# Kernel optimization log

Measured on AMD Instinct MI355X. Metric: run time of the kernel, lower is better.

The kernel has to match this reference:

```python
import jax, jax.numpy as jnp
import numpy as np

# V:N:M sparsity config (n=2 kept of m=8 per vector-block; mask pattern [1,0,1,0,0,0,0,0])
M_BLK = 8
KEEP_OFFSETS = np.array([0, 2], dtype=np.int32)  # positions kept in each m-block
B, S, D_IN, D_OUT = 2, 8192, 4096, 4096
K_KEPT = D_IN // M_BLK * len(KEEP_OFFSETS)  # 1024


def _keep_idx():
    # column indices of the surviving weight entries (same for every output row)
    blocks = np.arange(D_IN // M_BLK, dtype=np.int32)[:, None] * M_BLK  # [D_IN/M,1]
    return jnp.asarray((blocks + KEEP_OFFSETS[None, :]).reshape(-1))   # [K_KEPT]


def setup_inputs() -> dict:
    key = jax.random.key(0)
    k1, k2, k3 = jax.random.split(key, 3)
    x = jax.random.normal(k1, (B, S, D_IN), dtype=jnp.float32)
    values = jax.random.normal(k2, (D_OUT, K_KEPT), dtype=jnp.float32) * 0.02
    bias = jax.random.normal(k3, (D_OUT,), dtype=jnp.float32) * 0.02
    return {"x": x, "values": values, "bias": bias}


def reference(x, values, bias):
    # Sparse SpMM: gather kept input features, dense GEMM with compressed values.
    # Equivalent to x @ (masked dense W).T + bias, without materializing W.
    keep = _keep_idx()               # [K_KEPT] int32, constant metadata
    xg = x[..., keep]                # [B,S,K_KEPT]
    out = jnp.einsum('bsk,nk->bsn', xg, values) + bias  # [B,S,D_OUT]
    return out
```

## Files before the change

kernel.cpp:

```cpp
#include <hip/hip_runtime.h>
#include <hip/hip_bf16.h>


#define M_TOTAL 16384
#define DIN     4096
#define KDIM    1024
#define NDIM    4096

typedef unsigned short u16;
typedef unsigned int   u32;
typedef __bf16 bf16x8 __attribute__((ext_vector_type(8)));
typedef float  f32x4  __attribute__((ext_vector_type(4)));

typedef const void __attribute__((address_space(1)))* gp_t;
typedef void __attribute__((address_space(3)))*       lp_t;

__device__ __forceinline__ u16 f2bf(float f) {
    u32 u = __float_as_uint(f);
    u += 0x7FFFu + ((u >> 16) & 1u);
    return (u16)(u >> 16);
}

__global__ void compact_x_kernel(const float* __restrict__ x,
                                 u32* __restrict__ xg, int nblk) {
    int i = blockIdx.x * blockDim.x + threadIdx.x;
    const int stride = gridDim.x * blockDim.x;
    for (; i < nblk; i += stride) {
        float4 v = *reinterpret_cast<const float4*>(x + (size_t)i * 8);
        xg[i] = (u32)f2bf(v.x) | ((u32)f2bf(v.z) << 16);
    }
}

__global__ void conv_vals_kernel(const float* __restrict__ v,
                                 uint2* __restrict__ vb, int n4) {
    int i = blockIdx.x * blockDim.x + threadIdx.x;
    const int stride = gridDim.x * blockDim.x;
    for (; i < n4; i += stride) {
        float4 f = *reinterpret_cast<const float4*>(v + (size_t)i * 4);
        uint2 o;
        o.x = (u32)f2bf(f.x) | ((u32)f2bf(f.y) << 16);
        o.y = (u32)f2bf(f.z) | ((u32)f2bf(f.w) << 16);
        vb[i] = o;
    }
}


#define LDSA(d, kh) (((d) * 2 + (kh)) * 16384)
#define LDSB(d, kh) (65536 + ((d) * 2 + (kh)) * 16384)

#define LOADA(d, kh, mh) { _Pragma("unroll") \
    for (int m_ = 0; m_ < 4; ++m_) \
        af[m_] = *(const bf16x8*)(lds + LDSA(d, kh) + (wr * 8 + (mh) * 4 + m_) * 1024 + fl_off); }

#define LOADB(d, kh) { _Pragma("unroll") \
    for (int n_ = 0; n_ < 4; ++n_) \
        bfr[n_] = *(const bf16x8*)(lds + LDSB(d, kh) + (wc * 4 + n_) * 1024 + fl_off); }

#define MFMA16(mh) { \
    __builtin_amdgcn_s_setprio(1); \
    _Pragma("unroll") for (int m_ = 0; m_ < 4; ++m_) \
    _Pragma("unroll") for (int n_ = 0; n_ < 4; ++n_) \
        acc[(mh) * 4 + m_][n_] = __builtin_amdgcn_mfma_f32_16x16x32_bf16( \
            af[m_], bfr[n_], acc[(mh) * 4 + m_][n_], 0, 0, 0); \
    __builtin_amdgcn_s_setprio(0); }

#define BAR() __builtin_amdgcn_s_barrier()
#define VMCNT6() asm volatile("s_waitcnt vmcnt(6)" ::: "memory")
#define VMCNT0() asm volatile("s_waitcnt vmcnt(0)" ::: "memory")

__global__ __launch_bounds__(512, 2) void gemm_kernel(
    const u16* __restrict__ A, const u16* __restrict__ Bv,
    const float* __restrict__ bias, float* __restrict__ C)
{
    __shared__ __align__(1024) char lds[131072];

    const int tid  = threadIdx.x;
    const int lane = tid & 63;
    const int wid  = tid >> 6;
    const int wr   = wid >> 2;
    const int wc   = wid & 3;
    const int lrow = lane & 15;
    const int lg   = lane >> 4;

    const int b   = blockIdx.x;
    const int swz = (b & 7) * 128 + (b >> 3);
    const int btm = swz >> 4;
    const int btn = swz & 15;

    const int st_r0 = wid * 16 + (lane >> 2);
    const int st_ck = ((lane & 3) * 8) ^ ((lane & 32) >> 1);
    const u16* Asrc = A  + (size_t)(btm * 256 + st_r0) * KDIM + st_ck;
    const u16* Bsrc = Bv + (size_t)(btn * 256 + st_r0) * KDIM + st_ck;
    const int dst0 = tid * 16;

    const int fl_off = lrow * 64 + ((lg * 16) ^ (((lrow >> 3) & 1) << 5));

    auto STAGE = [&](int s) {
        const int kt = s >> 2, j = s & 3;
        const int d = kt & 1, kh = (j >> 1) & 1;
        const int ko = kt * 64 + kh * 32;
        const u16* src = (j & 1) ? Bsrc : Asrc;
        const int base = ((j & 1) ? 65536 : 0) + (d * 2 + kh) * 16384;
        __builtin_amdgcn_global_load_lds((gp_t)(src + ko),
            (lp_t)(lds + base + dst0), 16, 0, 0);
        __builtin_amdgcn_global_load_lds((gp_t)(src + 128 * KDIM + ko),
            (lp_t)(lds + base + 8192 + dst0), 16, 0, 0);
    };

    f32x4 acc[8][4] = {};
    bf16x8 af[4], bfr[4];

    STAGE(0); STAGE(1); STAGE(2); STAGE(3); STAGE(4); STAGE(5); STAGE(6);
    VMCNT6();
    BAR();

#pragma unroll 1
    for (int t = 0; t < 7; ++t) {
        const int s0 = 8 * t + 7;
        LOADB(0, 0); LOADA(0, 0, 0); STAGE(s0);     BAR(); MFMA16(0); BAR();
        LOADA(0, 0, 1);              STAGE(s0 + 1); BAR(); MFMA16(1); BAR();
        LOADB(0, 1); LOADA(0, 1, 0); STAGE(s0 + 2); BAR(); MFMA16(0); BAR();
        LOADA(0, 1, 1);              STAGE(s0 + 3); BAR(); MFMA16(1);
        VMCNT6(); BAR();
        LOADB(1, 0); LOADA(1, 0, 0); STAGE(s0 + 4); BAR(); MFMA16(0); BAR();
        LOADA(1, 0, 1);              STAGE(s0 + 5); BAR(); MFMA16(1); BAR();
        LOADB(1, 1); LOADA(1, 1, 0); STAGE(s0 + 6); BAR(); MFMA16(0); BAR();
        LOADA(1, 1, 1);              STAGE(s0 + 7); BAR(); MFMA16(1);
        VMCNT6(); BAR();
    }
    LOADB(0, 0); LOADA(0, 0, 0); STAGE(63);         BAR(); MFMA16(0); BAR();
    LOADA(0, 0, 1);                                 BAR(); MFMA16(1); BAR();
    LOADB(0, 1); LOADA(0, 1, 0);                    BAR(); MFMA16(0); BAR();
    LOADA(0, 1, 1);                                 BAR(); MFMA16(1);
    VMCNT0(); BAR();
    LOADB(1, 0); LOADA(1, 0, 0);                    BAR(); MFMA16(0); BAR();
    LOADA(1, 0, 1);                                 BAR(); MFMA16(1); BAR();
    LOADB(1, 1); LOADA(1, 1, 0);                    BAR(); MFMA16(0); BAR();
    LOADA(1, 1, 1);                                 BAR(); MFMA16(1);

    const int c_row0 = btm * 256 + wr * 128 + lg * 4;
    const int c_col0 = btn * 256 + wc * 64 + lrow;
    float bv[4];
#pragma unroll
    for (int n = 0; n < 4; ++n) bv[n] = bias[c_col0 + n * 16];
#pragma unroll
    for (int mi = 0; mi < 8; ++mi) {
        const int row = c_row0 + (mi >> 2) * 64 + (mi & 3) * 16;
#pragma unroll
        for (int n = 0; n < 4; ++n) {
#pragma unroll
            for (int j = 0; j < 4; ++j)
                C[(size_t)(row + j) * NDIM + c_col0 + n * 16] = acc[mi][n][j] + bv[n];
        }
    }
}

extern "C" void kernel_launch(void* const* d_in, const int* in_sizes, int n_in,
                              void* d_out, int out_size, void* d_ws, size_t ws_size,
                              hipStream_t stream) {
    const float* x      = (const float*)d_in[0];
    const float* values = (const float*)d_in[1];
    const float* bias   = (const float*)d_in[2];
    float* out = (float*)d_out;

    u16* xg = (u16*)d_ws;
    u16* vb = (u16*)((char*)d_ws + ((size_t)32 << 20));

    const int nblk = M_TOTAL * (DIN / 8);
    compact_x_kernel<<<2048, 256, 0, stream>>>(x, (u32*)xg, nblk);

    const int n4 = NDIM * KDIM / 4;
    conv_vals_kernel<<<1024, 256, 0, stream>>>(values, (uint2*)vb, n4);

    const int grid = (M_TOTAL / 256) * (NDIM / 256);
    gemm_kernel<<<grid, 512, 0, stream>>>(xg, vb, bias, out);
}
```

Baseline: 245.4 us.

## Make GEMM persistent over four M-tiles with cross-tile prefetch and merge prep kernels

The GEMM grid shrinks to 256 blocks, and each block loops over four 256-row M tiles that share one N tile. The first K stages of the next tile are prefetched while the current tile's tail MFMAs run, which removes the pipeline drain and refill between tiles. The bias load is hoisted out of the tile loop. The two conversion kernels are merged into one launch with wider 16-byte stores and more work per thread. The cost is one block per CU slot with no tail balancing, and output stores now sit between tiles and may stall the pipeline.

```diff
diff --git a/kernel.cpp b/kernel.cpp
--- a/kernel.cpp
+++ b/kernel.cpp
@@ -20,27 +20,37 @@
     u += 0x7FFFu + ((u >> 16) & 1u);
     return (u16)(u >> 16);
 }
-
-__global__ void compact_x_kernel(const float* __restrict__ x,
-                                 u32* __restrict__ xg, int nblk) {
-    int i = blockIdx.x * blockDim.x + threadIdx.x;
-    const int stride = gridDim.x * blockDim.x;
-    for (; i < nblk; i += stride) {
-        float4 v = *reinterpret_cast<const float4*>(x + (size_t)i * 8);
-        xg[i] = (u32)f2bf(v.x) | ((u32)f2bf(v.z) << 16);
-    }
+__device__ __forceinline__ u32 pack2(float a, float b) {
+    return (u32)f2bf(a) | ((u32)f2bf(b) << 16);
 }
 
-__global__ void conv_vals_kernel(const float* __restrict__ v,
-                                 uint2* __restrict__ vb, int n4) {
-    int i = blockIdx.x * blockDim.x + threadIdx.x;
-    const int stride = gridDim.x * blockDim.x;
-    for (; i < n4; i += stride) {
-        float4 f = *reinterpret_cast<const float4*>(v + (size_t)i * 4);
-        uint2 o;
-        o.x = (u32)f2bf(f.x) | ((u32)f2bf(f.y) << 16);
-        o.y = (u32)f2bf(f.z) | ((u32)f2bf(f.w) << 16);
-        vb[i] = o;
+__global__ void prep_kernel(const float* __restrict__ x, uint4* __restrict__ xg4,
+                            const float* __restrict__ vals, uint4* __restrict__ vb4) {
+    const int tid = threadIdx.x;
+    if (blockIdx.x < 2048) {
+        int i = blockIdx.x * 256 + tid;
+        const int stride = 2048 * 256;
+#pragma unroll
+        for (int it = 0; it < 4; ++it, i += stride) {
+            const float* p = x + (size_t)i * 32;
+            float4 a = *(const float4*)p;
+            float4 b = *(const float4*)(p + 8);
+            float4 c = *(const float4*)(p + 16);
+            float4 d = *(const float4*)(p + 24);
+            xg4[i] = make_uint4(pack2(a.x, a.z), pack2(b.x, b.z),
+                                pack2(c.x, c.z), pack2(d.x, d.z));
+        }
+    } else {
+        int i = (blockIdx.x - 2048) * 256 + tid;
+        const int stride = 256 * 256;
+#pragma unroll
+        for (int it = 0; it < 8; ++it, i += stride) {
+            const float* p = vals + (size_t)i * 8;
+            float4 a = *(const float4*)p;
+            float4 b = *(const float4*)(p + 4);
+            vb4[i] = make_uint4(pack2(a.x, a.y), pack2(a.z, a.w),
+                                pack2(b.x, b.y), pack2(b.z, b.w));
+        }
     }
 }
 
@@ -66,7 +76,6 @@
 
 #define BAR() __builtin_amdgcn_s_barrier()
 #define VMCNT6() asm volatile("s_waitcnt vmcnt(6)" ::: "memory")
-#define VMCNT0() asm volatile("s_waitcnt vmcnt(0)" ::: "memory")
 
 __global__ __launch_bounds__(512, 2) void gemm_kernel(
     const u16* __restrict__ A, const u16* __restrict__ Bv,
@@ -82,24 +91,23 @@
     const int lrow = lane & 15;
     const int lg   = lane >> 4;
 
-    const int b   = blockIdx.x;
-    const int swz = (b & 7) * 128 + (b >> 3);
-    const int btm = swz >> 4;
-    const int btn = swz & 15;
+    const int bb   = blockIdx.x;
+    const int btm0 = (bb & 7) * 8 + (bb >> 7);
+    const int btn  = (bb >> 3) & 15;
 
     const int st_r0 = wid * 16 + (lane >> 2);
     const int st_ck = ((lane & 3) * 8) ^ ((lane & 32) >> 1);
-    const u16* Asrc = A  + (size_t)(btm * 256 + st_r0) * KDIM + st_ck;
-    const u16* Bsrc = Bv + (size_t)(btn * 256 + st_r0) * KDIM + st_ck;
+    const u16* A0  = A  + (size_t)(btm0 * 256 + st_r0) * KDIM + st_ck;
+    const u16* Bs0 = Bv + (size_t)(btn  * 256 + st_r0) * KDIM + st_ck;
     const int dst0 = tid * 16;
 
     const int fl_off = lrow * 64 + ((lg * 16) ^ (((lrow >> 3) & 1) << 5));
 
-    auto STAGE = [&](int s) {
+    auto STAGE = [&](const u16* as_, int s) {
         const int kt = s >> 2, j = s & 3;
         const int d = kt & 1, kh = (j >> 1) & 1;
         const int ko = kt * 64 + kh * 32;
-        const u16* src = (j & 1) ? Bsrc : Asrc;
+        const u16* src = (j & 1) ? Bs0 : as_;
         const int base = ((j & 1) ? 65536 : 0) + (d * 2 + kh) * 16384;
         __builtin_amdgcn_global_load_lds((gp_t)(src + ko),
             (lp_t)(lds + base + dst0), 16, 0, 0);
@@ -107,50 +115,60 @@
             (lp_t)(lds + base + 8192 + dst0), 16, 0, 0);
     };
 
+    const int c_col0 = btn * 256 + wc * 64 + lrow;
+    float bvr[4];
+#pragma unroll
+    for (int n = 0; n < 4; ++n) bvr[n] = bias[c_col0 + n * 16];
+
     f32x4 acc[8][4] = {};
     bf16x8 af[4], bfr[4];
 
-    STAGE(0); STAGE(1); STAGE(2); STAGE(3); STAGE(4); STAGE(5); STAGE(6);
+    STAGE(A0, 0); STAGE(A0, 1); STAGE(A0, 2); STAGE(A0, 3);
+    STAGE(A0, 4); STAGE(A0, 5); STAGE(A0, 6);
     VMCNT6();
     BAR();
 
 #pragma unroll 1
-    for (int t = 0; t < 7; ++t) {
-        const int s0 = 8 * t + 7;
-        LOADB(0, 0); LOADA(0, 0, 0); STAGE(s0);     BAR(); MFMA16(0); BAR();
-        LOADA(0, 0, 1);              STAGE(s0 + 1); BAR(); MFMA16(1); BAR();
-        LOADB(0, 1); LOADA(0, 1, 0); STAGE(s0 + 2); BAR(); MFMA16(0); BAR();
-        LOADA(0, 1, 1);              STAGE(s0 + 3); BAR(); MFMA16(1);
+    for (int r = 0; r < 4; ++r) {
+        const u16* Ar = A0 + (size_t)r * 512 * KDIM;
+        const u16* An = (r < 3) ? (Ar + 512 * KDIM) : Ar;
+
+#pragma unroll 1
+        for (int t = 0; t < 7; ++t) {
+            const int s0 = 8 * t + 7;
+            LOADB(0, 0); LOADA(0, 0, 0); STAGE(Ar, s0);     BAR(); MFMA16(0); BAR();
+            LOADA(0, 0, 1);              STAGE(Ar, s0 + 1); BAR(); MFMA16(1); BAR();
+            LOADB(0, 1); LOADA(0, 1, 0); STAGE(Ar, s0 + 2); BAR(); MFMA16(0); BAR();
+            LOADA(0, 1, 1);              STAGE(Ar, s0 + 3); BAR(); MFMA16(1);
+            VMCNT6(); BAR();
+            LOADB(1, 0); LOADA(1, 0, 0); STAGE(Ar, s0 + 4); BAR(); MFMA16(0); BAR();
+            LOADA(1, 0, 1);              STAGE(Ar, s0 + 5); BAR(); MFMA16(1); BAR();
+            LOADB(1, 1); LOADA(1, 1, 0); STAGE(Ar, s0 + 6); BAR(); MFMA16(0); BAR();
+            LOADA(1, 1, 1);              STAGE(Ar, s0 + 7); BAR(); MFMA16(1);
+            VMCNT6(); BAR();
+        }
+        LOADB(0, 0); LOADA(0, 0, 0); STAGE(Ar, 63); BAR(); MFMA16(0); BAR();
+        LOADA(0, 0, 1);              STAGE(An, 0);  BAR(); MFMA16(1); BAR();
+        LOADB(0, 1); LOADA(0, 1, 0); STAGE(An, 1);  BAR(); MFMA16(0); BAR();
+        LOADA(0, 1, 1);              STAGE(An, 2);  BAR(); MFMA16(1);
         VMCNT6(); BAR();
-        LOADB(1, 0); LOADA(1, 0, 0); STAGE(s0 + 4); BAR(); MFMA16(0); BAR();
-        LOADA(1, 0, 1);              STAGE(s0 + 5); BAR(); MFMA16(1); BAR();
-        LOADB(1, 1); LOADA(1, 1, 0); STAGE(s0 + 6); BAR(); MFMA16(0); BAR();
-        LOADA(1, 1, 1);              STAGE(s0 + 7); BAR(); MFMA16(1);
+        LOADB(1, 0); LOADA(1, 0, 0); STAGE(An, 3);  BAR(); MFMA16(0); BAR();
+        LOADA(1, 0, 1);              STAGE(An, 4);  BAR(); MFMA16(1); BAR();
+        LOADB(1, 1); LOADA(1, 1, 0); STAGE(An, 5);  BAR(); MFMA16(0); BAR();
+        LOADA(1, 1, 1);              STAGE(An, 6);  BAR(); MFMA16(1);
         VMCNT6(); BAR();
-    }
-    LOADB(0, 0); LOADA(0, 0, 0); STAGE(63);         BAR(); MFMA16(0); BAR();
-    LOADA(0, 0, 1);                                 BAR(); MFMA16(1); BAR();
-    LOADB(0, 1); LOADA(0, 1, 0);                    BAR(); MFMA16(0); BAR();
-    LOADA(0, 1, 1);                                 BAR(); MFMA16(1);
-    VMCNT0(); BAR();
-    LOADB(1, 0); LOADA(1, 0, 0);                    BAR(); MFMA16(0); BAR();
-    LOADA(1, 0, 1);                                 BAR(); MFMA16(1); BAR();
-    LOADB(1, 1); LOADA(1, 1, 0);                    BAR(); MFMA16(0); BAR();
-    LOADA(1, 1, 1);                                 BAR(); MFMA16(1);
 
-    const int c_row0 = btm * 256 + wr * 128 + lg * 4;
-    const int c_col0 = btn * 256 + wc * 64 + lrow;
-    float bv[4];
+        const int c_row0 = (btm0 + 2 * r) * 256 + wr * 128 + lg * 4;
 #pragma unroll
-    for (int n = 0; n < 4; ++n) bv[n] = bias[c_col0 + n * 16];
+        for (int mi = 0; mi < 8; ++mi) {
+            const int row = c_row0 + (mi >> 2) * 64 + (mi & 3) * 16;
 #pragma unroll
-    for (int mi = 0; mi < 8; ++mi) {
-        const int row = c_row0 + (mi >> 2) * 64 + (mi & 3) * 16;
+            for (int n = 0; n < 4; ++n) {
 #pragma unroll
-        for (int n = 0; n < 4; ++n) {
-#pragma unroll
-            for (int j = 0; j < 4; ++j)
-                C[(size_t)(row + j) * NDIM + c_col0 + n * 16] = acc[mi][n][j] + bv[n];
+                for (int j = 0; j < 4; ++j)
+                    C[(size_t)(row + j) * NDIM + c_col0 + n * 16] = acc[mi][n][j] + bvr[n];
+                acc[mi][n] = (f32x4){0.f, 0.f, 0.f, 0.f};
+            }
         }
     }
 }
@@ -166,12 +184,6 @@
     u16* xg = (u16*)d_ws;
     u16* vb = (u16*)((char*)d_ws + ((size_t)32 << 20));
 
-    const int nblk = M_TOTAL * (DIN / 8);
-    compact_x_kernel<<<2048, 256, 0, stream>>>(x, (u32*)xg, nblk);
-
-    const int n4 = NDIM * KDIM / 4;
-    conv_vals_kernel<<<1024, 256, 0, stream>>>(values, (uint2*)vb, n4);
-
-    const int grid = (M_TOTAL / 256) * (NDIM / 256);
-    gemm_kernel<<<grid, 512, 0, stream>>>(xg, vb, bias, out);
+    prep_kernel<<<2304, 256, 0, stream>>>(x, (uint4*)xg, values, (uint4*)vb);
+    gemm_kernel<<<256, 512, 0, stream>>>(xg, vb, bias, out);
 }
```

New measurement: 226.4 us. -7.8%, faster.
